# Optimization experiments

Hardware: AMD Instinct MI355X
Metric: run time of the kernel (lower is better)

Reference implementation:

```python
import jax, jax.numpy as jnp
import numpy as np
import math

V, D, H, NL, L, B = 32000, 1024, 16, 6, 1024, 2
HD = D // H
EPS = 1e-5


def _positional(L, D):
    # matches torch: exp(arange(0,D,2) * -(log(1000)/D))
    div = jnp.exp(jnp.arange(0, D, 2, dtype=jnp.float32) * (-math.log(1000.0) / D))
    k = jnp.arange(L, dtype=jnp.float32)[:, None]
    pos = jnp.zeros((L, D), dtype=jnp.float32)
    pos = pos.at[:, 0::2].set(jnp.sin(k * div))
    pos = pos.at[:, 1::2].set(jnp.cos(k * div))
    return pos[None]  # [1, L, D]


def setup_inputs() -> dict:
    key = jax.random.key(0)
    ks = jax.random.split(key, 12)
    s = 0.02
    tokens = jax.random.randint(ks[0], (B, L), 0, V)
    emb = jax.random.normal(ks[1], (V, D), jnp.float32) * s
    pos = _positional(L, D)
    ln1_g = jnp.ones((NL, D), jnp.float32)
    ln1_b = jnp.zeros((NL, D), jnp.float32)
    ln2_g = jnp.ones((NL, D), jnp.float32)
    ln2_b = jnp.zeros((NL, D), jnp.float32)
    attn_w = jax.random.normal(ks[2], (NL, D, 3 * D), jnp.float32) * s
    attn_b = jnp.zeros((NL, 3 * D), jnp.float32)
    proj_w = jax.random.normal(ks[3], (NL, D, D), jnp.float32) * s
    proj_b = jnp.zeros((NL, D), jnp.float32)
    mlp_w1 = jax.random.normal(ks[4], (NL, D, 4 * D), jnp.float32) * s
    mlp_b1 = jnp.zeros((NL, 4 * D), jnp.float32)
    mlp_w2 = jax.random.normal(ks[5], (NL, 4 * D, D), jnp.float32) * s
    mlp_b2 = jnp.zeros((NL, D), jnp.float32)
    out_w = jax.random.normal(ks[6], (D, V), jnp.float32) * s
    return dict(tokens=tokens, pos=pos, emb=emb,
                ln1_g=ln1_g, ln1_b=ln1_b, ln2_g=ln2_g, ln2_b=ln2_b,
                attn_w=attn_w, attn_b=attn_b, proj_w=proj_w, proj_b=proj_b,
                mlp_w1=mlp_w1, mlp_b1=mlp_b1, mlp_w2=mlp_w2, mlp_b2=mlp_b2,
                out_w=out_w)


def _ln(x, g, b):
    mu = jnp.mean(x, -1, keepdims=True)
    var = jnp.mean(jnp.square(x - mu), -1, keepdims=True)
    return (x - mu) * jax.lax.rsqrt(var + EPS) * g + b


def _block(x, p, causal_mask):
    ln1_g, ln1_b, ln2_g, ln2_b, aw, ab, pw, pb, w1, b1, w2, b2 = p
    h = _ln(x, ln1_g, ln1_b)
    qkv = h @ aw + ab                      # [B, L, 3D]
    q, k, v = jnp.split(qkv, 3, axis=-1)
    Bc, Lc = x.shape[0], x.shape[1]
    q = q.reshape(Bc, Lc, H, HD)
    k = k.reshape(Bc, Lc, H, HD)
    v = v.reshape(Bc, Lc, H, HD)
    scores = jnp.einsum('blhd,bmhd->bhlm', q, k) * (1.0 / math.sqrt(HD))
    scores = jnp.where(causal_mask, scores, -jnp.inf)
    attn = jax.nn.softmax(scores, axis=-1)
    y = jnp.einsum('bhlm,bmhd->blhd', attn, v).reshape(Bc, Lc, D)
    x = x + (y @ pw + pb)
    r = _ln(x, ln2_g, ln2_b)
    # NOTE: original ModuleList order applies GELU AFTER the second linear
    r = jax.nn.gelu((r @ w1 + b1) @ w2 + b2, approximate=False)
    return x + r


def reference(tokens, pos, emb, ln1_g, ln1_b, ln2_g, ln2_b,
              attn_w, attn_b, proj_w, proj_b,
              mlp_w1, mlp_b1, mlp_w2, mlp_b2, out_w):
    x = emb[tokens] + pos                  # [B, L, D]
    Lc = x.shape[1]
    causal_mask = jnp.tril(jnp.ones((Lc, Lc), bool))[None, None]
    for i in range(NL):
        p = (ln1_g[i], ln1_b[i], ln2_g[i], ln2_b[i],
             attn_w[i], attn_b[i], proj_w[i], proj_b[i],
             mlp_w1[i], mlp_b1[i], mlp_w2[i], mlp_b2[i])
        x = _block(x, p, causal_mask)
    return x @ out_w                       # [B, L, V] logits
```

## Files before the change

kernel.cpp:

```cpp
#include <hip/hip_runtime.h>
#include <hip/hip_bf16.h>
#include <math.h>

typedef __bf16 bf16;
typedef __bf16 bf16x4 __attribute__((ext_vector_type(4)));
typedef __bf16 bf16x8 __attribute__((ext_vector_type(8)));
typedef float f32x4 __attribute__((ext_vector_type(4)));

__device__ __forceinline__ void gld_lds16(const void* g, void* l) {
    __builtin_amdgcn_global_load_lds(
        (const __attribute__((address_space(1))) unsigned int*)g,
        (__attribute__((address_space(3))) unsigned int*)l, 16, 0, 0);
}

#define VMW(n) asm volatile("s_waitcnt vmcnt(" #n ")" ::: "memory")
#define BARR() asm volatile("s_barrier" ::: "memory")

__global__ __launch_bounds__(256) void k_embed(const int* __restrict__ tok,
                                               const float* __restrict__ emb,
                                               const float* __restrict__ pos,
                                               float* __restrict__ x) {
    int row = blockIdx.x;
    int l = row & 1023;
    int tk = tok[row];
    const float4* e = (const float4*)(emb + (size_t)tk * 1024);
    const float4* p = (const float4*)(pos + (size_t)l * 1024);
    float4* o = (float4*)(x + (size_t)row * 1024);
    float4 a = e[threadIdx.x], b = p[threadIdx.x];
    o[threadIdx.x] = make_float4(a.x + b.x, a.y + b.y, a.z + b.z, a.w + b.w);
}

__global__ __launch_bounds__(256) void k_ln(const float* __restrict__ x,
                                            const float* __restrict__ g,
                                            const float* __restrict__ b,
                                            bf16* __restrict__ out) {
    int row = blockIdx.x;
    int t = threadIdx.x;
    const float4* xr = (const float4*)(x + (size_t)row * 1024);
    float4 v = xr[t];
    float s1 = v.x + v.y + v.z + v.w;
    float s2 = v.x * v.x + v.y * v.y + v.z * v.z + v.w * v.w;
#pragma unroll
    for (int o = 32; o; o >>= 1) { s1 += __shfl_down(s1, o); s2 += __shfl_down(s2, o); }
    __shared__ float ps1[4], ps2[4], stat[2];
    int lane = t & 63, wid = t >> 6;
    if (lane == 0) { ps1[wid] = s1; ps2[wid] = s2; }
    __syncthreads();
    if (t == 0) {
        float a1 = ps1[0] + ps1[1] + ps1[2] + ps1[3];
        float a2 = ps2[0] + ps2[1] + ps2[2] + ps2[3];
        float mu = a1 * (1.f / 1024.f);
        float var = a2 * (1.f / 1024.f) - mu * mu;
        stat[0] = mu; stat[1] = rsqrtf(var + 1e-5f);
    }
    __syncthreads();
    float mu = stat[0], rs = stat[1];
    const float4* gv = (const float4*)g;
    const float4* bv = (const float4*)b;
    float4 gg = gv[t], bb = bv[t];
    bf16x4 o4;
    o4[0] = (bf16)((v.x - mu) * rs * gg.x + bb.x);
    o4[1] = (bf16)((v.y - mu) * rs * gg.y + bb.y);
    o4[2] = (bf16)((v.z - mu) * rs * gg.z + bb.z);
    o4[3] = (bf16)((v.w - mu) * rs * gg.w + bb.w);
    *(bf16x4*)(out + (size_t)row * 1024 + t * 4) = o4;
}

__global__ __launch_bounds__(256) void k_cast(const float* __restrict__ x, bf16* __restrict__ o) {
    int i = blockIdx.x * 256 + threadIdx.x;
    float4 v = ((const float4*)x)[i];
    bf16x4 b;
    b[0] = (bf16)v.x; b[1] = (bf16)v.y; b[2] = (bf16)v.z; b[3] = (bf16)v.w;
    ((bf16x4*)o)[i] = b;
}

__device__ __forceinline__ void transpose64(const float* __restrict__ W,
                                            bf16* __restrict__ WT,
                                            int K, int N, int n0, int k0, int t,
                                            float (*tile)[65]) {
    int tx = t & 15, ty = t >> 4;
#pragma unroll
    for (int i = 0; i < 64; i += 16) {
        float4 v = *(const float4*)&W[(size_t)(k0 + ty + i) * N + n0 + tx * 4];
        tile[ty + i][tx * 4 + 0] = v.x;
        tile[ty + i][tx * 4 + 1] = v.y;
        tile[ty + i][tx * 4 + 2] = v.z;
        tile[ty + i][tx * 4 + 3] = v.w;
    }
    __syncthreads();
    int n = t >> 3, ks = t & 7;
#pragma unroll
    for (int pass = 0; pass < 2; ++pass) {
        int nn = n + pass * 32;
        bf16x8 v;
#pragma unroll
        for (int j = 0; j < 8; ++j) v[j] = (bf16)tile[ks * 8 + j][nn];
        *(bf16x8*)&WT[(size_t)(n0 + nn) * K + k0 + ks * 8] = v;
    }
}

__global__ __launch_bounds__(256) void k_transpose_layer(const float* __restrict__ aw,
                                                         const float* __restrict__ pw,
                                                         const float* __restrict__ m1,
                                                         const float* __restrict__ m2,
                                                         bf16* __restrict__ wT) {
    __shared__ float tile[64][65];
    int bid = blockIdx.x;
    const float* src; bf16* dst; int K, N, tn, tk;
    if (bid < 768)       { src = aw; dst = wT;            K = 1024; N = 3072; tn = bid % 48; tk = bid / 48; }
    else if (bid < 1024) { int b = bid - 768;  src = pw; dst = wT + 3145728; K = 1024; N = 1024; tn = b % 16; tk = b / 16; }
    else if (bid < 2048) { int b = bid - 1024; src = m1; dst = wT + 4194304; K = 1024; N = 4096; tn = b % 64; tk = b / 64; }
    else                 { int b = bid - 2048; src = m2; dst = wT + 8388608; K = 4096; N = 1024; tn = b % 16; tk = b / 16; }
    transpose64(src, dst, K, N, tn * 64, tk * 64, threadIdx.x, tile);
}

__global__ __launch_bounds__(256) void k_transpose_out(const float* __restrict__ W,
                                                       bf16* __restrict__ WT) {
    __shared__ float tile[64][65];
    int bid = blockIdx.x;
    int tn = bid % 500, tk = bid / 500;
    transpose64(W, WT, 1024, 32000, tn * 64, tk * 64, threadIdx.x, tile);
}

__device__ __forceinline__ void stage128(const char* Ab, const char* Bb,
                                         char* As, char* Bs, int Kb, int k0b, int t) {
#pragma unroll
    for (int j = 0; j < 4; ++j) {
        int idx = j * 256 + t;
        int row = idx >> 3;
        int cb = (idx & 7) << 4;
        int scb = cb ^ ((row & 7) << 4);
        gld_lds16(Ab + (size_t)row * Kb + k0b + scb, As + idx * 16);
        gld_lds16(Bb + (size_t)row * Kb + k0b + scb, Bs + idx * 16);
    }
}

template <int EPI>
__global__ __launch_bounds__(256) void k_gemm2(const bf16* __restrict__ A,
                                               const bf16* __restrict__ BT,
                                               const float* __restrict__ bias,
                                               const float* __restrict__ resid,
                                               float* __restrict__ outf,
                                               bf16* __restrict__ outb,
                                               int N, int K) {
    __shared__ __align__(16) bf16 As[2][128 * 64];
    __shared__ __align__(16) bf16 Bs[2][128 * 64];
    int per = gridDim.x >> 3;
    int tile = (blockIdx.x & 7) * per + (blockIdx.x >> 3);
    int bm = tile & 15, bn = tile >> 4;
    int t = threadIdx.x, lane = t & 63;
    int wr = t >> 7, wc = (t >> 6) & 1;
    f32x4 acc[4][4] = {};
    const char* Ab = (const char*)(A + (size_t)bm * 128 * K);
    const char* Bb = (const char*)(BT + (size_t)bn * 128 * K);
    int Kb = K * 2;
    int nk = K >> 6;
    stage128(Ab, Bb, (char*)As[0], (char*)Bs[0], Kb, 0, t);
    VMW(0); BARR();
    for (int tt = 0; tt < nk; ++tt) {
        int cur = tt & 1;
        if (tt + 1 < nk)
            stage128(Ab, Bb, (char*)As[cur ^ 1], (char*)Bs[cur ^ 1], Kb, (tt + 1) * 128, t);
        const char* Ac = (const char*)As[cur];
        const char* Bc = (const char*)Bs[cur];
#pragma unroll
        for (int kk = 0; kk < 2; ++kk) {
            bf16x8 af[4], bfr[4];
            int cb = kk * 64 + ((lane >> 4) << 4);
#pragma unroll
            for (int m = 0; m < 4; ++m) {
                int r = wr * 64 + m * 16 + (lane & 15);
                af[m] = *(const bf16x8*)(Ac + r * 128 + (cb ^ ((r & 7) << 4)));
            }
#pragma unroll
            for (int n = 0; n < 4; ++n) {
                int r = wc * 64 + n * 16 + (lane & 15);
                bfr[n] = *(const bf16x8*)(Bc + r * 128 + (cb ^ ((r & 7) << 4)));
            }
#pragma unroll
            for (int m = 0; m < 4; ++m)
#pragma unroll
                for (int n = 0; n < 4; ++n)
                    acc[m][n] = __builtin_amdgcn_mfma_f32_16x16x32_bf16(af[m], bfr[n], acc[m][n], 0, 0, 0);
        }
        VMW(0); BARR();
    }
    int row0 = bm * 128 + wr * 64 + ((lane >> 4) << 2);
    int col0 = bn * 128 + wc * 64 + (lane & 15);
#pragma unroll
    for (int m = 0; m < 4; ++m) {
#pragma unroll
        for (int n = 0; n < 4; ++n) {
            int col = col0 + n * 16;
            float bv = bias[col];
#pragma unroll
            for (int r = 0; r < 4; ++r) {
                int row = row0 + m * 16 + r;
                size_t idx = (size_t)row * N + col;
                float v = acc[m][n][r] + bv;
                if (EPI == 0) {
                    outb[idx] = (bf16)v;
                } else if (EPI == 1) {
                    outf[idx] = resid[idx] + v;
                } else {
                    outf[idx] = resid[idx] + 0.5f * v * (1.0f + erff(v * 0.70710678118f));
                }
            }
        }
    }
}

__device__ __forceinline__ void stage64(const char* Ab, const char* Bb,
                                        char* As, char* Bs, int Kb, int k0b, int t) {
#pragma unroll
    for (int j = 0; j < 2; ++j) {
        int idx = j * 256 + t;
        int row = idx >> 3;
        int cb = (idx & 7) << 4;
        int scb = cb ^ ((row & 7) << 4);
        gld_lds16(Ab + (size_t)row * Kb + k0b + scb, As + idx * 16);
        gld_lds16(Bb + (size_t)row * Kb + k0b + scb, Bs + idx * 16);
    }
}

template <int EPI>
__global__ __launch_bounds__(256) void k_gemm64(const bf16* __restrict__ A,
                                                const bf16* __restrict__ BT,
                                                const float* __restrict__ bias,
                                                const float* __restrict__ resid,
                                                float* __restrict__ outf,
                                                int N, int K) {
    __shared__ __align__(16) bf16 As[2][64 * 64];
    __shared__ __align__(16) bf16 Bs[2][64 * 64];
    int per = gridDim.x >> 3;
    int tile = (blockIdx.x & 7) * per + (blockIdx.x >> 3);
    int bm = tile & 31, bn = tile >> 5;
    int t = threadIdx.x, lane = t & 63, wid = t >> 6;
    f32x4 acc[4] = {};
    const char* Ab = (const char*)(A + (size_t)bm * 64 * K);
    const char* Bb = (const char*)(BT + (size_t)bn * 64 * K);
    int Kb = K * 2;
    int nk = K >> 6;
    stage64(Ab, Bb, (char*)As[0], (char*)Bs[0], Kb, 0, t);
    VMW(0); BARR();
    for (int tt = 0; tt < nk; ++tt) {
        int cur = tt & 1;
        if (tt + 1 < nk)
            stage64(Ab, Bb, (char*)As[cur ^ 1], (char*)Bs[cur ^ 1], Kb, (tt + 1) * 128, t);
        const char* Ac = (const char*)As[cur];
        const char* Bc = (const char*)Bs[cur];
#pragma unroll
        for (int kk = 0; kk < 2; ++kk) {
            int cb = kk * 64 + ((lane >> 4) << 4);
            int ra = wid * 16 + (lane & 15);
            bf16x8 af = *(const bf16x8*)(Ac + ra * 128 + (cb ^ ((ra & 7) << 4)));
            bf16x8 bfr[4];
#pragma unroll
            for (int n = 0; n < 4; ++n) {
                int r = n * 16 + (lane & 15);
                bfr[n] = *(const bf16x8*)(Bc + r * 128 + (cb ^ ((r & 7) << 4)));
            }
#pragma unroll
            for (int n = 0; n < 4; ++n)
                acc[n] = __builtin_amdgcn_mfma_f32_16x16x32_bf16(af, bfr[n], acc[n], 0, 0, 0);
        }
        VMW(0); BARR();
    }
    int row0 = bm * 64 + wid * 16 + ((lane >> 4) << 2);
    int col0 = bn * 64 + (lane & 15);
#pragma unroll
    for (int n = 0; n < 4; ++n) {
        int col = col0 + n * 16;
        float bv = bias[col];
#pragma unroll
        for (int r = 0; r < 4; ++r) {
            int row = row0 + r;
            size_t idx = (size_t)row * N + col;
            float v = acc[n][r] + bv;
            if (EPI == 1) {
                outf[idx] = resid[idx] + v;
            } else {
                outf[idx] = resid[idx] + 0.5f * v * (1.0f + erff(v * 0.70710678118f));
            }
        }
    }
}

__device__ __forceinline__ void stage_full256(const char* gtile, char* ldst,
                                              int Kb, int t) {
#pragma unroll
    for (int j = 0; j < 4; ++j) {
        int idx = j * 512 + t;
        int row = idx >> 3;
        int cb = (idx & 7) << 4;
        int scb = cb ^ ((row & 7) << 4);
        gld_lds16(gtile + (size_t)row * Kb + scb, ldst + idx * 16);
    }
}

template <int MH, int NH>
__device__ __forceinline__ void phase256(const bf16* Abuf, const bf16* Bbuf,
                                         int lane, int wm, int wn,
                                         f32x4 (&acc)[8][4]) {
    int lrow = lane & 15, lk = lane >> 4;
    bf16x8 af[4][2], bfr[2][2];
#pragma unroll
    for (int kk = 0; kk < 2; ++kk) {
        int cb = kk * 64 + lk * 16;
#pragma unroll
        for (int m = 0; m < 4; ++m) {
            int row = (MH * 4 + m) * 32 + wm * 16 + lrow;
            af[m][kk] = *(const bf16x8*)((const char*)Abuf + row * 128 + (cb ^ ((row & 7) << 4)));
        }
#pragma unroll
        for (int n = 0; n < 2; ++n) {
            int row = (NH * 2 + n) * 64 + wn * 16 + lrow;
            bfr[n][kk] = *(const bf16x8*)((const char*)Bbuf + row * 128 + (cb ^ ((row & 7) << 4)));
        }
    }
    __builtin_amdgcn_s_setprio(1);
#pragma unroll
    for (int kk = 0; kk < 2; ++kk)
#pragma unroll
        for (int m = 0; m < 4; ++m)
#pragma unroll
            for (int n = 0; n < 2; ++n)
                acc[MH * 4 + m][NH * 2 + n] = __builtin_amdgcn_mfma_f32_16x16x32_bf16(
                    af[m][kk], bfr[n][kk], acc[MH * 4 + m][NH * 2 + n], 0, 0, 0);
    __builtin_amdgcn_s_setprio(0);
    __builtin_amdgcn_sched_barrier(0);
}

__global__ __launch_bounds__(512, 1) void k_gemm256(const bf16* __restrict__ A,
                                                    const bf16* __restrict__ BT,
                                                    float* __restrict__ outf,
                                                    int N, int K) {
    __shared__ __align__(16) bf16 Asb[2][256 * 64];
    __shared__ __align__(16) bf16 Bsb[3][256 * 64];
    int t = threadIdx.x, lane = t & 63, wid = t >> 6;
    int wm = wid >> 2, wn = wid & 3;
    int tile = (blockIdx.x & 7) * 125 + (blockIdx.x >> 3);
    int bm = tile & 7;
    int bn = tile >> 3;

    const char* Ab = (const char*)(A + (size_t)bm * 256 * K);
    const char* Bb = (const char*)(BT + (size_t)bn * 256 * K);
    int Kb = K * 2;
    int nk = K >> 6;
    f32x4 acc[8][4] = {};

    stage_full256(Ab, (char*)Asb[0], Kb, t);
    stage_full256(Bb, (char*)Bsb[0], Kb, t);
    stage_full256(Bb + 128, (char*)Bsb[1], Kb, t);
    VMW(4);
    BARR();

    for (int tt = 0; tt < nk; ++tt) {
        BARR();
        int ka = (tt + 1 < nk) ? tt + 1 : nk - 1;
        int kb = (tt + 2 < nk) ? tt + 2 : nk - 1;
        stage_full256(Ab + (size_t)ka * 128, (char*)Asb[(tt + 1) & 1], Kb, t);
        stage_full256(Bb + (size_t)kb * 128, (char*)Bsb[(tt + 2) % 3], Kb, t);
        VMW(12);
        BARR();
        const bf16* Ac = Asb[tt & 1];
        const bf16* Bc = Bsb[tt % 3];
        phase256<0, 0>(Ac, Bc, lane, wm, wn, acc);
        phase256<0, 1>(Ac, Bc, lane, wm, wn, acc);
        phase256<1, 0>(Ac, Bc, lane, wm, wn, acc);
        phase256<1, 1>(Ac, Bc, lane, wm, wn, acc);
    }

    size_t row0 = (size_t)bm * 256 + wm * 16 + (lane >> 4) * 4;
    int col0 = bn * 256 + wn * 16 + (lane & 15);
#pragma unroll
    for (int mi = 0; mi < 8; ++mi) {
#pragma unroll
        for (int ni = 0; ni < 4; ++ni) {
            int col = col0 + ni * 64;
#pragma unroll
            for (int r = 0; r < 4; ++r) {
                size_t row = row0 + mi * 32 + r;
                outf[row * N + col] = acc[mi][ni][r];
            }
        }
    }
}

__global__ __launch_bounds__(256) void k_attn(const bf16* __restrict__ qkv, bf16* __restrict__ y) {
    int tile = (blockIdx.x & 7) * 64 + (blockIdx.x >> 3);
    int qb = tile & 15;
    int bh = tile >> 4;
    int b = bh >> 4, h = bh & 15;
    int t = threadIdx.x, lane = t & 63, wid = t >> 6;
    int tok0 = b << 10;
    int q0 = qb << 6;
    __shared__ bf16 Qs[64][64];
    __shared__ bf16 Ks[64][64];
    __shared__ bf16 Vt[64][64];
    __shared__ bf16 Ps[4][16][64];
    const char* qbase = (const char*)qkv;
#pragma unroll
    for (int j = 0; j < 2; ++j) {
        int off = (j * 256 + t) * 16;
        int row = off >> 7, colb = off & 127;
        gld_lds16(qbase + ((size_t)(tok0 + q0 + row) * 3072 + h * 64) * 2 + colb, (char*)Qs + off);
    }
    asm volatile("s_waitcnt vmcnt(0)" ::: "memory");
    __syncthreads();
    int kof = (lane >> 4) << 3;
    bf16x8 aq0 = *(const bf16x8*)&Qs[wid * 16 + (lane & 15)][kof];
    bf16x8 aq1 = *(const bf16x8*)&Qs[wid * 16 + (lane & 15)][32 + kof];
    f32x4 o[4] = {};
    float mrun[4], lrun[4];
#pragma unroll
    for (int r = 0; r < 4; ++r) { mrun[r] = -INFINITY; lrun[r] = 0.f; }
    int qrow = q0 + wid * 16 + ((lane >> 4) << 2);

    for (int kv0 = 0; kv0 <= q0; kv0 += 64) {
        __syncthreads();
#pragma unroll
        for (int j = 0; j < 2; ++j) {
            int off = (j * 256 + t) * 16;
            int row = off >> 7, colb = off & 127;
            gld_lds16(qbase + ((size_t)(tok0 + kv0 + row) * 3072 + 1024 + h * 64) * 2 + colb,
                      (char*)Ks + off);
        }
        {
            int kv = t >> 2, d0 = (t & 3) * 16;
            const bf16* vrow = qkv + (size_t)(tok0 + kv0 + kv) * 3072 + 2048 + h * 64 + d0;
#pragma unroll
            for (int e4 = 0; e4 < 4; ++e4) {
                bf16x4 vv = *(const bf16x4*)(vrow + e4 * 4);
                Vt[d0 + e4 * 4 + 0][kv] = vv[0];
                Vt[d0 + e4 * 4 + 1][kv] = vv[1];
                Vt[d0 + e4 * 4 + 2][kv] = vv[2];
                Vt[d0 + e4 * 4 + 3][kv] = vv[3];
            }
        }
        asm volatile("s_waitcnt vmcnt(0)" ::: "memory");
        __syncthreads();
        f32x4 s[4];
#pragma unroll
        for (int n = 0; n < 4; ++n) {
            bf16x8 bk0 = *(const bf16x8*)&Ks[n * 16 + (lane & 15)][kof];
            bf16x8 bk1 = *(const bf16x8*)&Ks[n * 16 + (lane & 15)][32 + kof];
            f32x4 z = {};
            z = __builtin_amdgcn_mfma_f32_16x16x32_bf16(aq0, bk0, z, 0, 0, 0);
            z = __builtin_amdgcn_mfma_f32_16x16x32_bf16(aq1, bk1, z, 0, 0, 0);
            s[n] = z;
        }
        float mx[4];
#pragma unroll
        for (int r = 0; r < 4; ++r) mx[r] = -INFINITY;
#pragma unroll
        for (int n = 0; n < 4; ++n) {
            int col = kv0 + n * 16 + (lane & 15);
#pragma unroll
            for (int r = 0; r < 4; ++r) {
                float sv = s[n][r] * 0.125f;
                sv = (col <= qrow + r) ? sv : -INFINITY;
                s[n][r] = sv;
                mx[r] = fmaxf(mx[r], sv);
            }
        }
#pragma unroll
        for (int r = 0; r < 4; ++r)
#pragma unroll
            for (int m = 1; m < 16; m <<= 1) mx[r] = fmaxf(mx[r], __shfl_xor(mx[r], m));
        float scl[4];
#pragma unroll
        for (int r = 0; r < 4; ++r) {
            float mn = fmaxf(mrun[r], mx[r]);
            scl[r] = __expf(mrun[r] - mn);
            mrun[r] = mn;
        }
        float rs[4] = {0.f, 0.f, 0.f, 0.f};
#pragma unroll
        for (int n = 0; n < 4; ++n)
#pragma unroll
            for (int r = 0; r < 4; ++r) {
                float p = __expf(s[n][r] - mrun[r]);
                s[n][r] = p;
                rs[r] += p;
            }
#pragma unroll
        for (int r = 0; r < 4; ++r) {
#pragma unroll
            for (int m = 1; m < 16; m <<= 1) rs[r] += __shfl_xor(rs[r], m);
            lrun[r] = lrun[r] * scl[r] + rs[r];
        }
#pragma unroll
        for (int n = 0; n < 4; ++n)
#pragma unroll
            for (int r = 0; r < 4; ++r) {
                o[n][r] *= scl[r];
                Ps[wid][(lane >> 4) * 4 + r][n * 16 + (lane & 15)] = (bf16)s[n][r];
            }
        bf16x8 ap0 = *(const bf16x8*)&Ps[wid][lane & 15][kof];
        bf16x8 ap1 = *(const bf16x8*)&Ps[wid][lane & 15][32 + kof];
#pragma unroll
        for (int n = 0; n < 4; ++n) {
            bf16x8 bv0 = *(const bf16x8*)&Vt[n * 16 + (lane & 15)][kof];
            bf16x8 bv1 = *(const bf16x8*)&Vt[n * 16 + (lane & 15)][32 + kof];
            o[n] = __builtin_amdgcn_mfma_f32_16x16x32_bf16(ap0, bv0, o[n], 0, 0, 0);
            o[n] = __builtin_amdgcn_mfma_f32_16x16x32_bf16(ap1, bv1, o[n], 0, 0, 0);
        }
    }
#pragma unroll
    for (int n = 0; n < 4; ++n)
#pragma unroll
        for (int r = 0; r < 4; ++r) {
            int row = tok0 + qrow + r;
            y[(size_t)row * 1024 + h * 64 + n * 16 + (lane & 15)] = (bf16)(o[n][r] / lrun[r]);
        }
}

extern "C" void kernel_launch(void* const* d_in, const int* in_sizes, int n_in,
                              void* d_out, int out_size, void* d_ws, size_t ws_size,
                              hipStream_t stream) {
    const int*   tokens = (const int*)d_in[0];
    const float* pos    = (const float*)d_in[1];
    const float* emb    = (const float*)d_in[2];
    const float* ln1_g  = (const float*)d_in[3];
    const float* ln1_b  = (const float*)d_in[4];
    const float* ln2_g  = (const float*)d_in[5];
    const float* ln2_b  = (const float*)d_in[6];
    const float* attn_w = (const float*)d_in[7];
    const float* attn_b = (const float*)d_in[8];
    const float* proj_w = (const float*)d_in[9];
    const float* proj_b = (const float*)d_in[10];
    const float* mlp_w1 = (const float*)d_in[11];
    const float* mlp_b1 = (const float*)d_in[12];
    const float* mlp_w2 = (const float*)d_in[13];
    const float* mlp_b2 = (const float*)d_in[14];
    const float* out_w  = (const float*)d_in[15];
    float* out = (float*)d_out;

    char* ws = (char*)d_ws;
    size_t off = 0;
    auto alloc = [&](size_t bytes) {
        void* p = ws + off;
        off = (off + bytes + 255) & ~(size_t)255;
        return p;
    };
    float* x   = (float*)alloc((size_t)2048 * 1024 * 4);
    bf16* hb   = (bf16*)alloc((size_t)2048 * 1024 * 2);
    bf16* qkvb = (bf16*)alloc((size_t)2048 * 3072 * 2);
    bf16* yb   = (bf16*)alloc((size_t)2048 * 1024 * 2);
    bf16* hidb = (bf16*)alloc((size_t)2048 * 4096 * 2);
    bf16* wT   = (bf16*)alloc((size_t)32000 * 1024 * 2);

    k_embed<<<2048, 256, 0, stream>>>(tokens, emb, pos, x);

    for (int i = 0; i < 6; ++i) {
        k_transpose_layer<<<3072, 256, 0, stream>>>(
            attn_w + (size_t)i * 1024 * 3072, proj_w + (size_t)i * 1024 * 1024,
            mlp_w1 + (size_t)i * 1024 * 4096, mlp_w2 + (size_t)i * 4096 * 1024, wT);
        k_ln<<<2048, 256, 0, stream>>>(x, ln1_g + i * 1024, ln1_b + i * 1024, hb);
        k_gemm2<0><<<384, 256, 0, stream>>>(hb, wT, attn_b + i * 3072,
                                            nullptr, nullptr, qkvb, 3072, 1024);
        k_attn<<<512, 256, 0, stream>>>(qkvb, yb);
        k_gemm64<1><<<512, 256, 0, stream>>>(yb, wT + 3145728, proj_b + i * 1024,
                                             x, x, 1024, 1024);
        k_ln<<<2048, 256, 0, stream>>>(x, ln2_g + i * 1024, ln2_b + i * 1024, hb);
        k_gemm2<0><<<512, 256, 0, stream>>>(hb, wT + 4194304, mlp_b1 + i * 4096,
                                            nullptr, nullptr, hidb, 4096, 1024);
        k_gemm64<2><<<512, 256, 0, stream>>>(hidb, wT + 8388608, mlp_b2 + i * 1024,
                                             x, x, 1024, 4096);
    }

    k_cast<<<2048, 256, 0, stream>>>(x, hb);
    k_transpose_out<<<8000, 256, 0, stream>>>(out_w, wT);
    k_gemm256<<<1000, 512, 0, stream>>>(hb, wT, out, 32000, 1024);
}
```

Measured before the change: 1.275 ms.

## Interleave global-to-LDS staging with MFMA phases in 256x256 GEMM main loop

```diff
diff --git a/kernel.cpp b/kernel.cpp
--- a/kernel.cpp
+++ b/kernel.cpp
@@ -298,26 +298,41 @@
     }
 }
 
+__device__ __forceinline__ void stage_half256(const char* gtile, char* ldst,
+                                              int Kb, int t, int half) {
+#pragma unroll
+    for (int j = 0; j < 2; ++j) {
+        int idx = (half * 2 + j) * 512 + t;
+        int row = idx >> 3;
+        int cb = (idx & 7) << 4;
+        int scb = cb ^ ((row & 7) << 4);
+        gld_lds16(gtile + (size_t)row * Kb + scb, ldst + idx * 16);
+    }
+}
+
 template <int MH, int NH>
-__device__ __forceinline__ void phase256(const bf16* Abuf, const bf16* Bbuf,
-                                         int lane, int wm, int wn,
-                                         f32x4 (&acc)[8][4]) {
-    int lrow = lane & 15, lk = lane >> 4;
-    bf16x8 af[4][2], bfr[2][2];
+__device__ __forceinline__ void phase_rd(const char* Ac, const char* Bc,
+                                         int lrow, int lk, int wm, int wn,
+                                         bf16x8 (&af)[4][2], bf16x8 (&bfr)[2][2]) {
 #pragma unroll
     for (int kk = 0; kk < 2; ++kk) {
         int cb = kk * 64 + lk * 16;
 #pragma unroll
         for (int m = 0; m < 4; ++m) {
             int row = (MH * 4 + m) * 32 + wm * 16 + lrow;
-            af[m][kk] = *(const bf16x8*)((const char*)Abuf + row * 128 + (cb ^ ((row & 7) << 4)));
+            af[m][kk] = *(const bf16x8*)(Ac + row * 128 + (cb ^ ((row & 7) << 4)));
         }
 #pragma unroll
         for (int n = 0; n < 2; ++n) {
             int row = (NH * 2 + n) * 64 + wn * 16 + lrow;
-            bfr[n][kk] = *(const bf16x8*)((const char*)Bbuf + row * 128 + (cb ^ ((row & 7) << 4)));
-        }
-    }
+            bfr[n][kk] = *(const bf16x8*)(Bc + row * 128 + (cb ^ ((row & 7) << 4)));
+        }
+    }
+}
+
+template <int MH, int NH>
+__device__ __forceinline__ void phase_mm(bf16x8 (&af)[4][2], bf16x8 (&bfr)[2][2],
+                                         f32x4 (&acc)[8][4]) {
     __builtin_amdgcn_s_setprio(1);
 #pragma unroll
     for (int kk = 0; kk < 2; ++kk)
@@ -339,6 +354,7 @@
     __shared__ __align__(16) bf16 Bsb[3][256 * 64];
     int t = threadIdx.x, lane = t & 63, wid = t >> 6;
     int wm = wid >> 2, wn = wid & 3;
+    int lrow = lane & 15, lk = lane >> 4;
     int tile = (blockIdx.x & 7) * 125 + (blockIdx.x >> 3);
     int bm = tile & 7;
     int bn = tile >> 3;
@@ -352,23 +368,38 @@
     stage_full256(Ab, (char*)Asb[0], Kb, t);
     stage_full256(Bb, (char*)Bsb[0], Kb, t);
     stage_full256(Bb + 128, (char*)Bsb[1], Kb, t);
-    VMW(4);
-    BARR();
 
     for (int tt = 0; tt < nk; ++tt) {
-        BARR();
         int ka = (tt + 1 < nk) ? tt + 1 : nk - 1;
         int kb = (tt + 2 < nk) ? tt + 2 : nk - 1;
-        stage_full256(Ab + (size_t)ka * 128, (char*)Asb[(tt + 1) & 1], Kb, t);
-        stage_full256(Bb + (size_t)kb * 128, (char*)Bsb[(tt + 2) % 3], Kb, t);
-        VMW(12);
-        BARR();
-        const bf16* Ac = Asb[tt & 1];
-        const bf16* Bc = Bsb[tt % 3];
-        phase256<0, 0>(Ac, Bc, lane, wm, wn, acc);
-        phase256<0, 1>(Ac, Bc, lane, wm, wn, acc);
-        phase256<1, 0>(Ac, Bc, lane, wm, wn, acc);
-        phase256<1, 1>(Ac, Bc, lane, wm, wn, acc);
+        const char* Ac = (const char*)Asb[tt & 1];
+        const char* Bc = (const char*)Bsb[tt % 3];
+        char* An = (char*)Asb[(tt + 1) & 1];
+        char* Bn = (char*)Bsb[(tt + 2) % 3];
+        const char* Ag = Ab + (size_t)ka * 128;
+        const char* Bg = Bb + (size_t)kb * 128;
+        VMW(4); BARR();
+        bf16x8 af[4][2], bfr[2][2];
+        phase_rd<0, 0>(Ac, Bc, lrow, lk, wm, wn, af, bfr);
+        stage_half256(Ag, An, Kb, t, 0);
+        BARR();
+        phase_mm<0, 0>(af, bfr, acc);
+        BARR();
+        phase_rd<0, 1>(Ac, Bc, lrow, lk, wm, wn, af, bfr);
+        stage_half256(Ag, An, Kb, t, 1);
+        BARR();
+        phase_mm<0, 1>(af, bfr, acc);
+        BARR();
+        phase_rd<1, 0>(Ac, Bc, lrow, lk, wm, wn, af, bfr);
+        stage_half256(Bg, Bn, Kb, t, 0);
+        BARR();
+        phase_mm<1, 0>(af, bfr, acc);
+        BARR();
+        phase_rd<1, 1>(Ac, Bc, lrow, lk, wm, wn, af, bfr);
+        stage_half256(Bg, Bn, Kb, t, 1);
+        BARR();
+        phase_mm<1, 1>(af, bfr, acc);
+        BARR();
     }
 
     size_t row0 = (size_t)bm * 256 + wm * 16 + (lane >> 4) * 4;
```

Result: no change. 1.269 ms (-0.5%).
